# Performance work log

Measured on AMD Instinct MI355X. Metric: run time of the kernel, lower is better.

## Reference

```python
import jax, jax.numpy as jnp
import numpy as np

V = 50000  # vocab (output_size)
H = 512    # hidden_size
SOS = 2


def gru_cell(x, h, Wih, Whh, bih, bhh):
    # Standard PyTorch GRUCell math. x,h: [B,H]; Wih,Whh: [3H,H]; biases: [3H]
    gx = x @ Wih.T + bih
    gh = h @ Whh.T + bhh
    gx_r, gx_z, gx_n = jnp.split(gx, 3, axis=-1)
    gh_r, gh_z, gh_n = jnp.split(gh, 3, axis=-1)
    r = jax.nn.sigmoid(gx_r + gh_r)
    z = jax.nn.sigmoid(gx_z + gh_z)
    n = jnp.tanh(gx_n + r * gh_n)
    return (1.0 - z) * n + z * h


def setup_inputs() -> dict:
    key = jax.random.key(0)
    ks = jax.random.split(key, 16)
    s = 1.0 / np.sqrt(H)
    u = lambda k, shp: jax.random.uniform(k, shp, jnp.float32, -s, s)
    return {
        "cw_idxs": jax.random.randint(ks[0], (32, 256), 0, V, jnp.int32),
        "qw_idxs": jax.random.randint(ks[1], (32, 32), 0, V, jnp.int32),
        "emb_enc": jax.random.normal(ks[2], (V, H), jnp.float32) * 0.02,
        "emb_dec": jax.random.normal(ks[3], (V, H), jnp.float32) * 0.02,
        "Wih_e": u(ks[4], (3 * H, H)), "Whh_e": u(ks[5], (3 * H, H)),
        "bih_e": u(ks[6], (3 * H,)), "bhh_e": u(ks[7], (3 * H,)),
        "Wih_d": u(ks[8], (3 * H, H)), "Whh_d": u(ks[9], (3 * H, H)),
        "bih_d": u(ks[10], (3 * H,)), "bhh_d": u(ks[11], (3 * H,)),
        "Wg": u(ks[12], (H, V)), "bg": u(ks[13], (V,)),
    }


def reference(cw_idxs, qw_idxs, emb_enc, emb_dec, Wih_e, Whh_e, bih_e, bhh_e,
              Wih_d, Whh_d, bih_d, bhh_d, Wg, bg):
    B, Tenc = cw_idxs.shape
    Tdec = qw_idxs.shape[1]

    # ---- Encoder: sequential GRU over context tokens ----
    enc_x = emb_enc[cw_idxs].transpose(1, 0, 2)  # [Tenc, B, H]
    h0 = jnp.zeros((B, H), jnp.float32)

    def enc_step(h, x_t):
        h = gru_cell(x_t, h, Wih_e, Whh_e, bih_e, bhh_e)
        return h, None

    h_enc, _ = jax.lax.scan(enc_step, h0, enc_x)

    # ---- Decoder with teacher forcing: input is SOS then shifted targets ----
    dec_in = jnp.concatenate(
        [jnp.full((B, 1), SOS, jnp.int32), qw_idxs[:, :-1]], axis=1)  # [B, Tdec]
    dec_x = jax.nn.relu(emb_dec[dec_in]).transpose(1, 0, 2)  # [Tdec, B, H]
    tgt = qw_idxs.T  # [Tdec, B]

    def dec_step(carry, inp):
        h, loss = carry
        x_t, y_t = inp
        h = gru_cell(x_t, h, Wih_d, Whh_d, bih_d, bhh_d)
        logp = jax.nn.log_softmax(h @ Wg + bg, axis=-1)  # [B, V]
        step_loss = -jnp.sum(jnp.take_along_axis(logp, y_t[:, None], axis=1))
        return (h, loss + step_loss), None

    (_, total_loss), _ = jax.lax.scan(
        dec_step, (h_enc, jnp.float32(0.0)), (dec_x, tgt))
    return total_loss / Tdec
```

## Files before the change

kernel.cpp:

```cpp
#include <hip/hip_runtime.h>
#include <math.h>

#define HH   512
#define BB   32
#define TENC 256
#define TDEC 32
#define VV   50000
#define SOSTOK 2
#define G3H  1536
#define NCG  49

__device__ __forceinline__ float sigmoidf_(float x) { return 1.0f / (1.0f + expf(-x)); }

__global__ __launch_bounds__(256) void transpose_w(
    const float* __restrict__ in, float* __restrict__ out)
{
    __shared__ float tile[32][33];
    const int kt = blockIdx.x * 32;
    const int jt = blockIdx.y * 32;
    const int tx = threadIdx.x & 31, ty = threadIdx.x >> 5;
#pragma unroll
    for (int l = 0; l < 4; l++) {
        int j = jt + ty + l * 8;
        tile[ty + l * 8][tx] = in[(size_t)j * HH + kt + tx];
    }
    __syncthreads();
#pragma unroll
    for (int l = 0; l < 4; l++) {
        int k = kt + ty + l * 8;
        out[(size_t)k * G3H + jt + tx] = tile[tx][ty + l * 8];
    }
}

__global__ __launch_bounds__(256) void transpose_w4(
    const float4* __restrict__ in, float4* __restrict__ out)
{
    __shared__ float4 tile[16][17];
    const int kt = blockIdx.x * 16;
    const int jt = blockIdx.y * 16;
    const int tx = threadIdx.x & 15, ty = threadIdx.x >> 4;
    tile[ty][tx] = in[(size_t)(jt + ty) * 128 + kt + tx];
    __syncthreads();
    out[(size_t)(kt + ty) * G3H + jt + tx] = tile[tx][ty];
}

__global__ __launch_bounds__(256) void gxT_kernel(
    const int* __restrict__ idxs, const float* __restrict__ emb,
    const float* __restrict__ WT, const float* __restrict__ bias,
    float* __restrict__ out, int dec_mode)
{
    __shared__ __align__(16) float As[16][HH];
    const int tid = threadIdx.x;
    const int m0 = blockIdx.x * 16;

    for (int l = tid; l < 16 * HH; l += 256) {
        int r = l >> 9, k = l & (HH - 1);
        int m = m0 + r;
        int t = m >> 5, b = m & 31;
        int idx;
        if (dec_mode) idx = (t == 0) ? SOSTOK : idxs[b * TDEC + (t - 1)];
        else          idx = idxs[b * TENC + t];
        float v = emb[(size_t)idx * HH + k];
        if (dec_mode) v = fmaxf(v, 0.0f);
        As[r][k] = v;
    }
    __syncthreads();

    const int j0 = blockIdx.y * 1024 + tid * 4;
    if (j0 >= G3H) return;

    float acc[16][4];
#pragma unroll
    for (int r = 0; r < 16; r++)
#pragma unroll
        for (int jj = 0; jj < 4; jj++) acc[r][jj] = 0.0f;

    for (int kc = 0; kc < HH; kc += 4) {
        float4 w0 = *(const float4*)(WT + (size_t)(kc + 0) * G3H + j0);
        float4 w1 = *(const float4*)(WT + (size_t)(kc + 1) * G3H + j0);
        float4 w2 = *(const float4*)(WT + (size_t)(kc + 2) * G3H + j0);
        float4 w3 = *(const float4*)(WT + (size_t)(kc + 3) * G3H + j0);
#pragma unroll
        for (int r = 0; r < 16; r++) {
            float4 a = *(const float4*)(&As[r][kc]);
            acc[r][0] += a.x * w0.x + a.y * w1.x + a.z * w2.x + a.w * w3.x;
            acc[r][1] += a.x * w0.y + a.y * w1.y + a.z * w2.y + a.w * w3.y;
            acc[r][2] += a.x * w0.z + a.y * w1.z + a.z * w2.z + a.w * w3.z;
            acc[r][3] += a.x * w0.w + a.y * w1.w + a.z * w2.w + a.w * w3.w;
        }
    }

    float4 bv = *(const float4*)(bias + j0);
#pragma unroll
    for (int r = 0; r < 16; r++) {
        float4 o;
        o.x = acc[r][0] + bv.x;
        o.y = acc[r][1] + bv.y;
        o.z = acc[r][2] + bv.z;
        o.w = acc[r][3] + bv.w;
        *(float4*)(out + (size_t)(m0 + r) * G3H + j0) = o;
    }
}

__global__ __launch_bounds__(256) void gru_step3(
    const float4* __restrict__ WT4,
    const float* __restrict__ bhh,
    const float* __restrict__ gx_t,
    const float* __restrict__ h_in,
    float* __restrict__ h_out)
{
    __shared__ float4 hs[512];
    const int tid = threadIdx.x;
    const int bid = blockIdx.x;
    const int bq = bid & 7;
    const int it = bid >> 3;
    const int bl = tid >> 6;
    const int lane = tid & 63;
    const int kq = lane >> 4;
    const int il = lane & 15;
    const int b = bq * 4 + bl;
    const int i = it * 16 + il;

    const float4* hin4 = (const float4*)h_in;
    hs[tid]       = hin4[bq * 512 + tid];
    hs[tid + 256] = hin4[bq * 512 + tid + 256];
    __syncthreads();

    const int k4base = kq * 32;
    const float4* hb = &hs[bl * 128 + k4base];
    const float4* wr = WT4 + (size_t)k4base * G3H + i;
    const float4* wz = wr + HH;
    const float4* wn = wr + 2 * HH;

    float ar = 0.f, az = 0.f, an = 0.f;
#pragma unroll 8
    for (int m = 0; m < 32; m++) {
        float4 h4 = hb[m];
        float4 w0 = wr[(size_t)m * G3H];
        float4 w1 = wz[(size_t)m * G3H];
        float4 w2 = wn[(size_t)m * G3H];
        ar += h4.x * w0.x + h4.y * w0.y + h4.z * w0.z + h4.w * w0.w;
        az += h4.x * w1.x + h4.y * w1.y + h4.z * w1.z + h4.w * w1.w;
        an += h4.x * w2.x + h4.y * w2.y + h4.z * w2.z + h4.w * w2.w;
    }

    ar += __shfl_xor(ar, 16); az += __shfl_xor(az, 16); an += __shfl_xor(an, 16);
    ar += __shfl_xor(ar, 32); az += __shfl_xor(az, 32); an += __shfl_xor(an, 32);

    if (kq == 0) {
        float r = sigmoidf_(gx_t[b * G3H + i]            + ar + bhh[i]);
        float z = sigmoidf_(gx_t[b * G3H + HH + i]       + az + bhh[HH + i]);
        float n = tanhf    (gx_t[b * G3H + 2 * HH + i]   + r * (an + bhh[2 * HH + i]));
        float hp = h_in[b * HH + i];
        h_out[b * HH + i] = (1.0f - z) * n + z * hp;
    }
}

__global__ __launch_bounds__(256) void logits_kernel(
    const float* __restrict__ Hall,
    const float* __restrict__ Wg,
    const float* __restrict__ bg,
    const int* __restrict__ qw,
    float* __restrict__ pmax,
    float* __restrict__ psum,
    float* __restrict__ tgt_logit)
{
    __shared__ __align__(16) float As[16][HH];
    __shared__ float wred[16][4];
    const int tid = threadIdx.x;
    const int m0 = blockIdx.x * 16;
    const int lane = tid & 63, wid = tid >> 6;

    for (int l = tid; l < 16 * HH; l += 256) {
        int r = l >> 9, k = l & (HH - 1);
        As[r][k] = Hall[(size_t)(m0 + r) * HH + k];
    }
    __syncthreads();

    const int j0 = blockIdx.y * 1024 + tid * 4;
    const bool valid = (j0 < VV);

    float acc[16][4];
#pragma unroll
    for (int r = 0; r < 16; r++)
#pragma unroll
        for (int jj = 0; jj < 4; jj++) acc[r][jj] = 0.0f;

    if (valid) {
        for (int kc = 0; kc < HH; kc += 4) {
            float4 w0 = *(const float4*)(Wg + (size_t)(kc + 0) * VV + j0);
            float4 w1 = *(const float4*)(Wg + (size_t)(kc + 1) * VV + j0);
            float4 w2 = *(const float4*)(Wg + (size_t)(kc + 2) * VV + j0);
            float4 w3 = *(const float4*)(Wg + (size_t)(kc + 3) * VV + j0);
#pragma unroll
            for (int r = 0; r < 16; r++) {
                float4 a = *(const float4*)(&As[r][kc]);
                acc[r][0] += a.x * w0.x + a.y * w1.x + a.z * w2.x + a.w * w3.x;
                acc[r][1] += a.x * w0.y + a.y * w1.y + a.z * w2.y + a.w * w3.y;
                acc[r][2] += a.x * w0.z + a.y * w1.z + a.z * w2.z + a.w * w3.z;
                acc[r][3] += a.x * w0.w + a.y * w1.w + a.z * w2.w + a.w * w3.w;
            }
        }
        float4 bv = *(const float4*)(bg + j0);
#pragma unroll
        for (int r = 0; r < 16; r++) {
            acc[r][0] += bv.x; acc[r][1] += bv.y; acc[r][2] += bv.z; acc[r][3] += bv.w;
        }
#pragma unroll
        for (int r = 0; r < 16; r++) {
            int m = m0 + r, t = m >> 5, b = m & 31;
            int tj = qw[b * TDEC + t];
            if (tj >= j0 && tj < j0 + 4) tgt_logit[m] = acc[r][tj - j0];
        }
    }

    float rowmax[16];
#pragma unroll
    for (int r = 0; r < 16; r++) {
        float v = valid ? fmaxf(fmaxf(acc[r][0], acc[r][1]), fmaxf(acc[r][2], acc[r][3]))
                        : -INFINITY;
        for (int off = 32; off > 0; off >>= 1) v = fmaxf(v, __shfl_xor(v, off));
        if (lane == 0) wred[r][wid] = v;
    }
    __syncthreads();
#pragma unroll
    for (int r = 0; r < 16; r++)
        rowmax[r] = fmaxf(fmaxf(wred[r][0], wred[r][1]), fmaxf(wred[r][2], wred[r][3]));
    __syncthreads();

#pragma unroll
    for (int r = 0; r < 16; r++) {
        float s = 0.0f;
        if (valid) {
            s = expf(acc[r][0] - rowmax[r]) + expf(acc[r][1] - rowmax[r])
              + expf(acc[r][2] - rowmax[r]) + expf(acc[r][3] - rowmax[r]);
        }
        for (int off = 32; off > 0; off >>= 1) s += __shfl_xor(s, off);
        if (lane == 0) wred[r][wid] = s;
    }
    __syncthreads();

    if (tid < 16) {
        int r = tid;
        float S = wred[r][0] + wred[r][1] + wred[r][2] + wred[r][3];
        pmax[blockIdx.y * 1024 + m0 + r] = rowmax[r];
        psum[blockIdx.y * 1024 + m0 + r] = S;
    }
}

__global__ __launch_bounds__(256) void loss_kernel(
    const float* __restrict__ pmax, const float* __restrict__ psum,
    const float* __restrict__ tgt_logit, float* __restrict__ out)
{
    const int tid = threadIdx.x;
    float local = 0.0f;
    for (int m = tid; m < 1024; m += 256) {
        float M = -INFINITY;
        for (int cg = 0; cg < NCG; cg++) M = fmaxf(M, pmax[cg * 1024 + m]);
        float S = 0.0f;
        for (int cg = 0; cg < NCG; cg++) S += psum[cg * 1024 + m] * expf(pmax[cg * 1024 + m] - M);
        local += M + logf(S) - tgt_logit[m];
    }
    __shared__ float red[256];
    red[tid] = local;
    __syncthreads();
    for (int s = 128; s > 0; s >>= 1) {
        if (tid < s) red[tid] += red[tid + s];
        __syncthreads();
    }
    if (tid == 0) out[0] = red[0] / (float)TDEC;
}

extern "C" void kernel_launch(void* const* d_in, const int* in_sizes, int n_in,
                              void* d_out, int out_size, void* d_ws, size_t ws_size,
                              hipStream_t stream)
{
    const int*   cw     = (const int*)  d_in[0];
    const int*   qw     = (const int*)  d_in[1];
    const float* emb_e  = (const float*)d_in[2];
    const float* emb_d  = (const float*)d_in[3];
    const float* Wih_e  = (const float*)d_in[4];
    const float* Whh_e  = (const float*)d_in[5];
    const float* bih_e  = (const float*)d_in[6];
    const float* bhh_e  = (const float*)d_in[7];
    const float* Wih_d  = (const float*)d_in[8];
    const float* Whh_d  = (const float*)d_in[9];
    const float* bih_d  = (const float*)d_in[10];
    const float* bhh_d  = (const float*)d_in[11];
    const float* Wg     = (const float*)d_in[12];
    const float* bg     = (const float*)d_in[13];

    float* ws      = (float*)d_ws;
    float* gx_enc  = ws;
    float* gx_dec  = gx_enc + (size_t)8192 * G3H;
    float* hbuf0   = gx_dec + (size_t)1024 * G3H;
    float* hbuf1   = hbuf0 + BB * HH;
    float* h_all   = hbuf1 + BB * HH;
    float* pmax    = h_all + (size_t)1024 * HH;
    float* psum    = pmax + NCG * 1024;
    float* tgt_l   = psum + NCG * 1024;
    float* WihT_e  = tgt_l + 1024;
    float* WihT_d  = WihT_e + (size_t)HH * G3H;
    float* WhhT4_e = WihT_d + (size_t)HH * G3H;
    float* WhhT4_d = WhhT4_e + (size_t)HH * G3H;

    hipMemsetAsync(hbuf0, 0, BB * HH * sizeof(float), stream);

    transpose_w <<<dim3(16, 48), 256, 0, stream>>>(Wih_e, WihT_e);
    transpose_w <<<dim3(16, 48), 256, 0, stream>>>(Wih_d, WihT_d);
    transpose_w4<<<dim3(8, 96),  256, 0, stream>>>((const float4*)Whh_e, (float4*)WhhT4_e);
    transpose_w4<<<dim3(8, 96),  256, 0, stream>>>((const float4*)Whh_d, (float4*)WhhT4_d);

    gxT_kernel<<<dim3(512, 2), 256, 0, stream>>>(cw, emb_e, WihT_e, bih_e, gx_enc, 0);

    for (int t = 0; t < TENC; t++) {
        const float* hin = (t & 1) ? hbuf1 : hbuf0;
        float*       hout = (t & 1) ? hbuf0 : hbuf1;
        gru_step3<<<256, 256, 0, stream>>>(
            (const float4*)WhhT4_e, bhh_e, gx_enc + (size_t)t * BB * G3H, hin, hout);
    }

    gxT_kernel<<<dim3(64, 2), 256, 0, stream>>>(qw, emb_d, WihT_d, bih_d, gx_dec, 1);

    for (int t = 0; t < TDEC; t++) {
        const float* hin = (t == 0) ? hbuf0 : h_all + (size_t)(t - 1) * BB * HH;
        gru_step3<<<256, 256, 0, stream>>>(
            (const float4*)WhhT4_d, bhh_d, gx_dec + (size_t)t * BB * G3H, hin,
            h_all + (size_t)t * BB * HH);
    }

    logits_kernel<<<dim3(64, NCG), 256, 0, stream>>>(h_all, Wg, bg, qw, pmax, psum, tgt_l);

    loss_kernel<<<1, 256, 0, stream>>>(pmax, psum, tgt_l, (float*)d_out);
}
```

Baseline: 4.118 ms.

## Fuse GRU recurrence into persistent kernel with LDS-resident weights and grid barrier

```diff
diff --git a/kernel.cpp b/kernel.cpp
--- a/kernel.cpp
+++ b/kernel.cpp
@@ -9,6 +9,7 @@
 #define SOSTOK 2
 #define G3H  1536
 #define NCG  49
+#define SCAN_NBLK 256
 
 __device__ __forceinline__ float sigmoidf_(float x) { return 1.0f / (1.0f + expf(-x)); }
 
@@ -32,28 +33,16 @@
     }
 }
 
-__global__ __launch_bounds__(256) void transpose_w4(
-    const float4* __restrict__ in, float4* __restrict__ out)
-{
-    __shared__ float4 tile[16][17];
-    const int kt = blockIdx.x * 16;
-    const int jt = blockIdx.y * 16;
-    const int tx = threadIdx.x & 15, ty = threadIdx.x >> 4;
-    tile[ty][tx] = in[(size_t)(jt + ty) * 128 + kt + tx];
-    __syncthreads();
-    out[(size_t)(kt + ty) * G3H + jt + tx] = tile[tx][ty];
-}
-
-__global__ __launch_bounds__(256) void gxT_kernel(
+__global__ __launch_bounds__(256, 2) void gxT_kernel(
     const int* __restrict__ idxs, const float* __restrict__ emb,
     const float* __restrict__ WT, const float* __restrict__ bias,
     float* __restrict__ out, int dec_mode)
 {
-    __shared__ __align__(16) float As[16][HH];
+    __shared__ __align__(16) float As[32][HH];
     const int tid = threadIdx.x;
-    const int m0 = blockIdx.x * 16;
-
-    for (int l = tid; l < 16 * HH; l += 256) {
+    const int m0 = blockIdx.x * 32;
+
+    for (int l = tid; l < 32 * HH; l += 256) {
         int r = l >> 9, k = l & (HH - 1);
         int m = m0 + r;
         int t = m >> 5, b = m & 31;
@@ -69,9 +58,9 @@
     const int j0 = blockIdx.y * 1024 + tid * 4;
     if (j0 >= G3H) return;
 
-    float acc[16][4];
-#pragma unroll
-    for (int r = 0; r < 16; r++)
+    float acc[32][4];
+#pragma unroll
+    for (int r = 0; r < 32; r++)
 #pragma unroll
         for (int jj = 0; jj < 4; jj++) acc[r][jj] = 0.0f;
 
@@ -81,7 +70,7 @@
         float4 w2 = *(const float4*)(WT + (size_t)(kc + 2) * G3H + j0);
         float4 w3 = *(const float4*)(WT + (size_t)(kc + 3) * G3H + j0);
 #pragma unroll
-        for (int r = 0; r < 16; r++) {
+        for (int r = 0; r < 32; r++) {
             float4 a = *(const float4*)(&As[r][kc]);
             acc[r][0] += a.x * w0.x + a.y * w1.x + a.z * w2.x + a.w * w3.x;
             acc[r][1] += a.x * w0.y + a.y * w1.y + a.z * w2.y + a.w * w3.y;
@@ -92,7 +81,7 @@
 
     float4 bv = *(const float4*)(bias + j0);
 #pragma unroll
-    for (int r = 0; r < 16; r++) {
+    for (int r = 0; r < 32; r++) {
         float4 o;
         o.x = acc[r][0] + bv.x;
         o.y = acc[r][1] + bv.y;
@@ -102,61 +91,132 @@
     }
 }
 
-__global__ __launch_bounds__(256) void gru_step3(
-    const float4* __restrict__ WT4,
-    const float* __restrict__ bhh,
+__device__ __forceinline__ void grid_sync(unsigned* bar)
+{
+    __syncthreads();
+    if (threadIdx.x == 0) {
+        __threadfence();
+        unsigned my = __hip_atomic_load(&bar[1], __ATOMIC_RELAXED, __HIP_MEMORY_SCOPE_AGENT);
+        unsigned prev = __hip_atomic_fetch_add(&bar[0], 1u, __ATOMIC_ACQ_REL, __HIP_MEMORY_SCOPE_AGENT);
+        if (prev == SCAN_NBLK - 1) {
+            __hip_atomic_store(&bar[0], 0u, __ATOMIC_RELAXED, __HIP_MEMORY_SCOPE_AGENT);
+            __hip_atomic_fetch_add(&bar[1], 1u, __ATOMIC_ACQ_REL, __HIP_MEMORY_SCOPE_AGENT);
+        } else {
+            while (__hip_atomic_load(&bar[1], __ATOMIC_RELAXED, __HIP_MEMORY_SCOPE_AGENT) == my)
+                __builtin_amdgcn_s_sleep(1);
+        }
+        __threadfence();
+    }
+    __syncthreads();
+}
+
+__device__ __forceinline__ void gru_step(
+    const float* __restrict__ wm,
+    const float* __restrict__ bh,
     const float* __restrict__ gx_t,
     const float* __restrict__ h_in,
-    float* __restrict__ h_out)
-{
-    __shared__ float4 hs[512];
+    float* __restrict__ h_out,
+    int b, int kq, int i0)
+{
+    float p0=0,p1=0,p2=0,p3=0,p4=0,p5=0,p6=0,p7=0;
+    if (kq == 0) {
+        p0 = gx_t[b * G3H + i0];          p1 = gx_t[b * G3H + i0 + 1];
+        p2 = gx_t[b * G3H + 512 + i0];    p3 = gx_t[b * G3H + 512 + i0 + 1];
+        p4 = gx_t[b * G3H + 1024 + i0];   p5 = gx_t[b * G3H + 1024 + i0 + 1];
+        p6 = h_in[b * HH + i0];           p7 = h_in[b * HH + i0 + 1];
+    }
+
+    const float* hp  = h_in + b * HH + kq * 64;
+    const float* w00 = wm + 0 * 544 + kq * 68;
+    const float* w01 = wm + 1 * 544 + kq * 68;
+    const float* w10 = wm + 2 * 544 + kq * 68;
+    const float* w11 = wm + 3 * 544 + kq * 68;
+    const float* w20 = wm + 4 * 544 + kq * 68;
+    const float* w21 = wm + 5 * 544 + kq * 68;
+
+    float ar0 = 0.f, ar1 = 0.f, az0 = 0.f, az1 = 0.f, an0 = 0.f, an1 = 0.f;
+#pragma unroll
+    for (int c = 0; c < 16; c++) {
+        float4 h4 = *(const float4*)(hp + c * 4);
+        float4 w;
+        w = *(const float4*)(w00 + c * 4); ar0 += h4.x*w.x + h4.y*w.y + h4.z*w.z + h4.w*w.w;
+        w = *(const float4*)(w01 + c * 4); ar1 += h4.x*w.x + h4.y*w.y + h4.z*w.z + h4.w*w.w;
+        w = *(const float4*)(w10 + c * 4); az0 += h4.x*w.x + h4.y*w.y + h4.z*w.z + h4.w*w.w;
+        w = *(const float4*)(w11 + c * 4); az1 += h4.x*w.x + h4.y*w.y + h4.z*w.z + h4.w*w.w;
+        w = *(const float4*)(w20 + c * 4); an0 += h4.x*w.x + h4.y*w.y + h4.z*w.z + h4.w*w.w;
+        w = *(const float4*)(w21 + c * 4); an1 += h4.x*w.x + h4.y*w.y + h4.z*w.z + h4.w*w.w;
+    }
+    ar0 += __shfl_xor(ar0, 1); ar0 += __shfl_xor(ar0, 2); ar0 += __shfl_xor(ar0, 4);
+    ar1 += __shfl_xor(ar1, 1); ar1 += __shfl_xor(ar1, 2); ar1 += __shfl_xor(ar1, 4);
+    az0 += __shfl_xor(az0, 1); az0 += __shfl_xor(az0, 2); az0 += __shfl_xor(az0, 4);
+    az1 += __shfl_xor(az1, 1); az1 += __shfl_xor(az1, 2); az1 += __shfl_xor(az1, 4);
+    an0 += __shfl_xor(an0, 1); an0 += __shfl_xor(an0, 2); an0 += __shfl_xor(an0, 4);
+    an1 += __shfl_xor(an1, 1); an1 += __shfl_xor(an1, 2); an1 += __shfl_xor(an1, 4);
+
+    if (kq == 0) {
+        float r0 = sigmoidf_(p0 + ar0 + bh[0]);
+        float z0 = sigmoidf_(p2 + az0 + bh[2]);
+        float n0 = tanhf    (p4 + r0 * (an0 + bh[4]));
+        h_out[b * HH + i0]     = (1.0f - z0) * n0 + z0 * p6;
+        float r1 = sigmoidf_(p1 + ar1 + bh[1]);
+        float z1 = sigmoidf_(p3 + az1 + bh[3]);
+        float n1 = tanhf    (p5 + r1 * (an1 + bh[5]));
+        h_out[b * HH + i0 + 1] = (1.0f - z1) * n1 + z1 * p7;
+    }
+}
+
+__global__ __launch_bounds__(256, 1) void scan_kernel(
+    const float* __restrict__ Whh_e, const float* __restrict__ bhh_e,
+    const float* __restrict__ Whh_d, const float* __restrict__ bhh_d,
+    const float* __restrict__ gx_enc, const float* __restrict__ gx_dec,
+    float* __restrict__ hb0, float* __restrict__ hb1,
+    float* __restrict__ h_all, unsigned* __restrict__ bar)
+{
+    __shared__ __align__(16) float wlds[2][6][544];
     const int tid = threadIdx.x;
     const int bid = blockIdx.x;
-    const int bq = bid & 7;
-    const int it = bid >> 3;
-    const int bl = tid >> 6;
-    const int lane = tid & 63;
-    const int kq = lane >> 4;
-    const int il = lane & 15;
-    const int b = bq * 4 + bl;
-    const int i = it * 16 + il;
-
-    const float4* hin4 = (const float4*)h_in;
-    hs[tid]       = hin4[bq * 512 + tid];
-    hs[tid + 256] = hin4[bq * 512 + tid + 256];
-    __syncthreads();
-
-    const int k4base = kq * 32;
-    const float4* hb = &hs[bl * 128 + k4base];
-    const float4* wr = WT4 + (size_t)k4base * G3H + i;
-    const float4* wz = wr + HH;
-    const float4* wn = wr + 2 * HH;
-
-    float ar = 0.f, az = 0.f, an = 0.f;
-#pragma unroll 8
-    for (int m = 0; m < 32; m++) {
-        float4 h4 = hb[m];
-        float4 w0 = wr[(size_t)m * G3H];
-        float4 w1 = wz[(size_t)m * G3H];
-        float4 w2 = wn[(size_t)m * G3H];
-        ar += h4.x * w0.x + h4.y * w0.y + h4.z * w0.z + h4.w * w0.w;
-        az += h4.x * w1.x + h4.y * w1.y + h4.z * w1.z + h4.w * w1.w;
-        an += h4.x * w2.x + h4.y * w2.y + h4.z * w2.z + h4.w * w2.w;
-    }
-
-    ar += __shfl_xor(ar, 16); az += __shfl_xor(az, 16); an += __shfl_xor(an, 16);
-    ar += __shfl_xor(ar, 32); az += __shfl_xor(az, 32); an += __shfl_xor(an, 32);
-
-    if (kq == 0) {
-        float r = sigmoidf_(gx_t[b * G3H + i]            + ar + bhh[i]);
-        float z = sigmoidf_(gx_t[b * G3H + HH + i]       + az + bhh[HH + i]);
-        float n = tanhf    (gx_t[b * G3H + 2 * HH + i]   + r * (an + bhh[2 * HH + i]));
-        float hp = h_in[b * HH + i];
-        h_out[b * HH + i] = (1.0f - z) * n + z * hp;
-    }
-}
-
-__global__ __launch_bounds__(256) void logits_kernel(
+    const int b   = tid >> 3;
+    const int kq  = tid & 7;
+    const int i0  = bid * 2;
+
+#pragma unroll
+    for (int m = 0; m < 2; m++) {
+        const float* W = m ? Whh_d : Whh_e;
+#pragma unroll
+        for (int g = 0; g < 3; g++)
+#pragma unroll
+            for (int il = 0; il < 2; il++) {
+                const float* src = W + (size_t)(g * 512 + i0 + il) * 512;
+                for (int k = tid; k < 512; k += 256)
+                    wlds[m][g * 2 + il][(k >> 6) * 68 + (k & 63)] = src[k];
+            }
+    }
+    float bhE[6], bhD[6];
+#pragma unroll
+    for (int g = 0; g < 3; g++)
+#pragma unroll
+        for (int il = 0; il < 2; il++) {
+            bhE[g * 2 + il] = bhh_e[g * 512 + i0 + il];
+            bhD[g * 2 + il] = bhh_d[g * 512 + i0 + il];
+        }
+    __syncthreads();
+
+    for (int t = 0; t < TENC; t++) {
+        const float* hin = (t & 1) ? hb1 : hb0;
+        float*       hout = (t & 1) ? hb0 : hb1;
+        gru_step(&wlds[0][0][0], bhE, gx_enc + (size_t)t * BB * G3H, hin, hout, b, kq, i0);
+        grid_sync(bar);
+    }
+
+    for (int t = 0; t < TDEC; t++) {
+        const float* hin = (t == 0) ? hb0 : (h_all + (size_t)(t - 1) * BB * HH);
+        float*       hout = h_all + (size_t)t * BB * HH;
+        gru_step(&wlds[1][0][0], bhD, gx_dec + (size_t)t * BB * G3H, hin, hout, b, kq, i0);
+        if (t < TDEC - 1) grid_sync(bar);
+    }
+}
+
+__global__ __launch_bounds__(256, 2) void logits_kernel(
     const float* __restrict__ Hall,
     const float* __restrict__ Wg,
     const float* __restrict__ bg,
@@ -165,13 +225,12 @@
     float* __restrict__ psum,
     float* __restrict__ tgt_logit)
 {
-    __shared__ __align__(16) float As[16][HH];
-    __shared__ float wred[16][4];
+    __shared__ __align__(16) float As[32][HH];
     const int tid = threadIdx.x;
-    const int m0 = blockIdx.x * 16;
+    const int m0 = blockIdx.x * 32;
     const int lane = tid & 63, wid = tid >> 6;
 
-    for (int l = tid; l < 16 * HH; l += 256) {
+    for (int l = tid; l < 32 * HH; l += 256) {
         int r = l >> 9, k = l & (HH - 1);
         As[r][k] = Hall[(size_t)(m0 + r) * HH + k];
     }
@@ -180,9 +239,9 @@
     const int j0 = blockIdx.y * 1024 + tid * 4;
     const bool valid = (j0 < VV);
 
-    float acc[16][4];
-#pragma unroll
-    for (int r = 0; r < 16; r++)
+    float acc[32][4];
+#pragma unroll
+    for (int r = 0; r < 32; r++)
 #pragma unroll
         for (int jj = 0; jj < 4; jj++) acc[r][jj] = 0.0f;
 
@@ -193,7 +252,7 @@
             float4 w2 = *(const float4*)(Wg + (size_t)(kc + 2) * VV + j0);
             float4 w3 = *(const float4*)(Wg + (size_t)(kc + 3) * VV + j0);
 #pragma unroll
-            for (int r = 0; r < 16; r++) {
+            for (int r = 0; r < 32; r++) {
                 float4 a = *(const float4*)(&As[r][kc]);
                 acc[r][0] += a.x * w0.x + a.y * w1.x + a.z * w2.x + a.w * w3.x;
                 acc[r][1] += a.x * w0.y + a.y * w1.y + a.z * w2.y + a.w * w3.y;
@@ -203,48 +262,55 @@
         }
         float4 bv = *(const float4*)(bg + j0);
 #pragma unroll
-        for (int r = 0; r < 16; r++) {
+        for (int r = 0; r < 32; r++) {
             acc[r][0] += bv.x; acc[r][1] += bv.y; acc[r][2] += bv.z; acc[r][3] += bv.w;
         }
 #pragma unroll
-        for (int r = 0; r < 16; r++) {
-            int m = m0 + r, t = m >> 5, b = m & 31;
-            int tj = qw[b * TDEC + t];
+        for (int r = 0; r < 32; r++) {
+            int m = m0 + r, t = m >> 5, bb = m & 31;
+            int tj = qw[bb * TDEC + t];
             if (tj >= j0 && tj < j0 + 4) tgt_logit[m] = acc[r][tj - j0];
         }
     }
 
-    float rowmax[16];
-#pragma unroll
-    for (int r = 0; r < 16; r++) {
+    __syncthreads();
+    float* wredf = &As[0][0];
+
+    float rowmax[32];
+#pragma unroll
+    for (int r = 0; r < 32; r++) {
         float v = valid ? fmaxf(fmaxf(acc[r][0], acc[r][1]), fmaxf(acc[r][2], acc[r][3]))
                         : -INFINITY;
         for (int off = 32; off > 0; off >>= 1) v = fmaxf(v, __shfl_xor(v, off));
-        if (lane == 0) wred[r][wid] = v;
-    }
-    __syncthreads();
-#pragma unroll
-    for (int r = 0; r < 16; r++)
-        rowmax[r] = fmaxf(fmaxf(wred[r][0], wred[r][1]), fmaxf(wred[r][2], wred[r][3]));
-    __syncthreads();
-
-#pragma unroll
-    for (int r = 0; r < 16; r++) {
+        if (lane == 0) wredf[r * 4 + wid] = v;
+    }
+    __syncthreads();
+#pragma unroll
+    for (int r = 0; r < 32; r++)
+        rowmax[r] = fmaxf(fmaxf(wredf[r * 4 + 0], wredf[r * 4 + 1]),
+                          fmaxf(wredf[r * 4 + 2], wredf[r * 4 + 3]));
+    if (tid == 0) {
+#pragma unroll
+        for (int r = 0; r < 32; r++) pmax[blockIdx.y * 1024 + m0 + r] = rowmax[r];
+    }
+    __syncthreads();
+
+#pragma unroll
+    for (int r = 0; r < 32; r++) {
         float s = 0.0f;
         if (valid) {
             s = expf(acc[r][0] - rowmax[r]) + expf(acc[r][1] - rowmax[r])
               + expf(acc[r][2] - rowmax[r]) + expf(acc[r][3] - rowmax[r]);
         }
         for (int off = 32; off > 0; off >>= 1) s += __shfl_xor(s, off);
-        if (lane == 0) wred[r][wid] = s;
-    }
-    __syncthreads();
-
-    if (tid < 16) {
-        int r = tid;
-        float S = wred[r][0] + wred[r][1] + wred[r][2] + wred[r][3];
-        pmax[blockIdx.y * 1024 + m0 + r] = rowmax[r];
-        psum[blockIdx.y * 1024 + m0 + r] = S;
+        if (lane == 0) wredf[r * 4 + wid] = s;
+    }
+    __syncthreads();
+
+    if (tid < 32) {
+        float S = wredf[tid * 4 + 0] + wredf[tid * 4 + 1]
+                + wredf[tid * 4 + 2] + wredf[tid * 4 + 3];
+        psum[blockIdx.y * 1024 + m0 + tid] = S;
     }
 }
 
@@ -301,35 +367,21 @@
     float* tgt_l   = psum + NCG * 1024;
     float* WihT_e  = tgt_l + 1024;
     float* WihT_d  = WihT_e + (size_t)HH * G3H;
-    float* WhhT4_e = WihT_d + (size_t)HH * G3H;
-    float* WhhT4_d = WhhT4_e + (size_t)HH * G3H;
+    unsigned* bar  = (unsigned*)(WihT_d + (size_t)HH * G3H);
 
     hipMemsetAsync(hbuf0, 0, BB * HH * sizeof(float), stream);
-
-    transpose_w <<<dim3(16, 48), 256, 0, stream>>>(Wih_e, WihT_e);
-    transpose_w <<<dim3(16, 48), 256, 0, stream>>>(Wih_d, WihT_d);
-    transpose_w4<<<dim3(8, 96),  256, 0, stream>>>((const float4*)Whh_e, (float4*)WhhT4_e);
-    transpose_w4<<<dim3(8, 96),  256, 0, stream>>>((const float4*)Whh_d, (float4*)WhhT4_d);
-
-    gxT_kernel<<<dim3(512, 2), 256, 0, stream>>>(cw, emb_e, WihT_e, bih_e, gx_enc, 0);
-
-    for (int t = 0; t < TENC; t++) {
-        const float* hin = (t & 1) ? hbuf1 : hbuf0;
-        float*       hout = (t & 1) ? hbuf0 : hbuf1;
-        gru_step3<<<256, 256, 0, stream>>>(
-            (const float4*)WhhT4_e, bhh_e, gx_enc + (size_t)t * BB * G3H, hin, hout);
-    }
-
-    gxT_kernel<<<dim3(64, 2), 256, 0, stream>>>(qw, emb_d, WihT_d, bih_d, gx_dec, 1);
-
-    for (int t = 0; t < TDEC; t++) {
-        const float* hin = (t == 0) ? hbuf0 : h_all + (size_t)(t - 1) * BB * HH;
-        gru_step3<<<256, 256, 0, stream>>>(
-            (const float4*)WhhT4_d, bhh_d, gx_dec + (size_t)t * BB * G3H, hin,
-            h_all + (size_t)t * BB * HH);
-    }
-
-    logits_kernel<<<dim3(64, NCG), 256, 0, stream>>>(h_all, Wg, bg, qw, pmax, psum, tgt_l);
+    hipMemsetAsync(bar, 0, 2 * sizeof(unsigned), stream);
+
+    transpose_w<<<dim3(16, 48), 256, 0, stream>>>(Wih_e, WihT_e);
+    transpose_w<<<dim3(16, 48), 256, 0, stream>>>(Wih_d, WihT_d);
+
+    gxT_kernel<<<dim3(256, 2), 256, 0, stream>>>(cw, emb_e, WihT_e, bih_e, gx_enc, 0);
+    gxT_kernel<<<dim3(32, 2),  256, 0, stream>>>(qw, emb_d, WihT_d, bih_d, gx_dec, 1);
+
+    scan_kernel<<<SCAN_NBLK, 256, 0, stream>>>(
+        Whh_e, bhh_e, Whh_d, bhh_d, gx_enc, gx_dec, hbuf0, hbuf1, h_all, bar);
+
+    logits_kernel<<<dim3(32, NCG), 256, 0, stream>>>(h_all, Wg, bg, qw, pmax, psum, tgt_l);
 
     loss_kernel<<<1, 256, 0, stream>>>(pmax, psum, tgt_l, (float*)d_out);
 }
```

After: 9.849 ms. +139.1%, slower.
